# Optimization experiments

Measured on AMD Instinct MI355X. Metric: run time of the kernel, lower is better.

## Reference

```python
import jax, jax.numpy as jnp
import numpy as np

B, S, D, H = 2, 2048, 1024, 16
DK = D // H
MAX_REL = 2047          # clip range for relative distances
REL_DIM = 64            # rel_embedding dim, summed over


def setup_inputs() -> dict:
    key = jax.random.key(0)
    ks = jax.random.split(key, 12)
    sc = 1.0 / np.sqrt(D)
    inp = {
        "q": jax.random.normal(ks[0], (B, S, D), jnp.float32),
        "k": jax.random.normal(ks[1], (B, S, D), jnp.float32),
        "v": jax.random.normal(ks[2], (B, S, D), jnp.float32),
        "Wq": jax.random.normal(ks[3], (D, D), jnp.float32) * sc,
        "bq": jnp.zeros((D,), jnp.float32),
        "Wk": jax.random.normal(ks[4], (D, D), jnp.float32) * sc,
        "bk": jnp.zeros((D,), jnp.float32),
        "Wv": jax.random.normal(ks[5], (D, D), jnp.float32) * sc,
        "bv": jnp.zeros((D,), jnp.float32),
        "Wo": jax.random.normal(ks[6], (D, D), jnp.float32) * sc,
        "bo": jnp.zeros((D,), jnp.float32),
        "rel_table": jax.random.normal(ks[7], (2 * MAX_REL + 1, REL_DIM), jnp.float32) * 0.02,
        "mask": jnp.tril(jnp.ones((1, 1, S, S), jnp.bool_)),  # causal
    }
    return inp


def reference(q, k, v, Wq, bq, Wk, bk, Wv, bv, Wo, bo, rel_table, mask):
    def split_heads(x):
        # [B,S,D] -> [B,H,S,DK]
        return x.reshape(B, -1, H, DK).transpose(0, 2, 1, 3)

    Q = split_heads(q @ Wq + bq)
    K = split_heads(k @ Wk + bk)
    V = split_heads(v @ Wv + bv)

    scores = jnp.einsum("bhqd,bhkd->bhqk", Q, K) / jnp.sqrt(jnp.float32(DK))

    # relative position bias: table[clip(j - i)] summed over rel dim -> [S,S]
    rel_idx = jnp.clip(jnp.arange(S)[None, :] - jnp.arange(S)[:, None],
                       -MAX_REL, MAX_REL) + MAX_REL
    rel_bias = rel_table[rel_idx].sum(-1)  # [S,S]
    scores = scores + rel_bias[None, None]

    scores = jnp.where(mask, scores, jnp.float32(-1e20))
    attn = jax.nn.softmax(scores, axis=-1)

    out = jnp.einsum("bhqk,bhkd->bhqd", attn, V)
    out = out.transpose(0, 2, 1, 3).reshape(B, -1, D)
    return out @ Wo + bo
```

## Files before the change

### kernel.cpp

```cpp
#include <hip/hip_runtime.h>

#define SEQ 2048
#define DIM 1024
#define NH 16
#define HD 64
#define NB 2

typedef __bf16 bf16x8 __attribute__((ext_vector_type(8)));
typedef float f32x4 __attribute__((ext_vector_type(4)));
typedef float f32x4v __attribute__((ext_vector_type(4)));
typedef float f32x4u __attribute__((ext_vector_type(4), aligned(4)));
typedef unsigned short us8 __attribute__((ext_vector_type(8)));
typedef unsigned short us4 __attribute__((ext_vector_type(4)));

#define LOG2E 1.44269504f

__device__ __forceinline__ unsigned short bfbits(float f) {
  __bf16 h = (__bf16)f;
  return __builtin_bit_cast(unsigned short, h);
}

__global__ void relsum_kernel(const float* __restrict__ rel_table,
                              float* __restrict__ relsum) {
  int i = blockIdx.x * blockDim.x + threadIdx.x;
  if (i < 4095) {
    const f32x4v* row = reinterpret_cast<const f32x4v*>(rel_table + (size_t)i * 64);
    float s = 0.f;
    for (int d = 0; d < 16; ++d) {
      f32x4v v = row[d];
      s += v[0] + v[1] + v[2] + v[3];
    }
    relsum[i] = s * LOG2E;
  }
}

__global__ __launch_bounds__(256) void wconv4_kernel(
    const float* __restrict__ W0, const float* __restrict__ W1,
    const float* __restrict__ W2, const float* __restrict__ W3,
    unsigned short* __restrict__ Wt) {
  __shared__ unsigned short T[64][68];
  int z = blockIdx.z;
  const float* W = (z == 0) ? W0 : (z == 1) ? W1 : (z == 2) ? W2 : W3;
  unsigned short* out = Wt + (size_t)z * 1024 * 1024;
  int r0 = blockIdx.y * 64;
  int c0 = blockIdx.x * 64;
  int tid = threadIdx.x;
  for (int it = 0; it < 4; ++it) {
    int s = tid + it * 256;
    int r = s >> 4;
    int c4 = (s & 15) * 4;
    f32x4v v = *reinterpret_cast<const f32x4v*>(W + (size_t)(r0 + r) * 1024 + c0 + c4);
    us4 o;
    o[0] = bfbits(v[0]); o[1] = bfbits(v[1]); o[2] = bfbits(v[2]); o[3] = bfbits(v[3]);
    *reinterpret_cast<us4*>(&T[r][c4]) = o;
  }
  __syncthreads();
  for (int it = 0; it < 2; ++it) {
    int s = tid + it * 256;
    int n = s >> 3;
    int k8 = (s & 7) * 8;
    us8 o;
    for (int e = 0; e < 8; ++e) o[e] = T[k8 + e][n];
    *reinterpret_cast<us8*>(out + (size_t)(c0 + n) * 1024 + r0 + k8) = o;
  }
}

template <int A_BF16, int OUT_BF16>
__global__ __launch_bounds__(256) void gemm_bias_kernel(
    const void* __restrict__ Ap, const unsigned short* __restrict__ WT,
    const float* __restrict__ bias, void* __restrict__ Cp, float oscale) {
  constexpr int N = 1024, K = 1024;
  int o = ((blockIdx.x & 7) << 6) | (blockIdx.x >> 3);
  int col0 = (o & 15) * 64;
  int row0 = (o >> 4) * 128;
  int tid = threadIdx.x;
  int w = tid >> 6;
  int lane = tid & 63;
  int lg = lane >> 4;
  int li = lane & 15;
  int wr = (w >> 1) * 64;
  int wc = (w & 1) * 32;

  __shared__ unsigned short As[128][72];
  __shared__ unsigned short Ws[64][72];

  f32x4 acc[4][2] = {};

  for (int k0 = 0; k0 < K; k0 += 64) {
    __syncthreads();
    if (A_BF16) {
      const unsigned short* A = (const unsigned short*)Ap;
      for (int it = 0; it < 4; ++it) {
        int s = tid + it * 256;
        int r = s >> 3;
        int cg = (s & 7) * 8;
        us8 vv = *reinterpret_cast<const us8*>(A + (size_t)(row0 + r) * K + k0 + cg);
        *reinterpret_cast<us8*>(&As[r][cg]) = vv;
      }
    } else {
      const float* A = (const float*)Ap;
      for (int it = 0; it < 8; ++it) {
        int s = tid + it * 256;
        int r = s >> 4;
        int cg = (s & 15) * 4;
        f32x4v vv = *reinterpret_cast<const f32x4v*>(A + (size_t)(row0 + r) * K + k0 + cg);
        us4 o2;
        o2[0] = bfbits(vv[0]); o2[1] = bfbits(vv[1]); o2[2] = bfbits(vv[2]); o2[3] = bfbits(vv[3]);
        *reinterpret_cast<us4*>(&As[r][cg]) = o2;
      }
    }
    for (int it = 0; it < 2; ++it) {
      int s = tid + it * 256;
      int c = s >> 3;
      int kg = (s & 7) * 8;
      us8 vv = *reinterpret_cast<const us8*>(WT + (size_t)(col0 + c) * K + k0 + kg);
      *reinterpret_cast<us8*>(&Ws[c][kg]) = vv;
    }
    __syncthreads();
    for (int kk = 0; kk < 2; ++kk) {
      bf16x8 af[4], bfr[2];
      for (int m = 0; m < 4; ++m)
        af[m] = *reinterpret_cast<const bf16x8*>(&As[wr + m * 16 + li][kk * 32 + lg * 8]);
      for (int n = 0; n < 2; ++n)
        bfr[n] = *reinterpret_cast<const bf16x8*>(&Ws[wc + n * 16 + li][kk * 32 + lg * 8]);
      for (int m = 0; m < 4; ++m)
        for (int n = 0; n < 2; ++n)
          acc[m][n] = __builtin_amdgcn_mfma_f32_16x16x32_bf16(af[m], bfr[n], acc[m][n], 0, 0, 0);
    }
  }

  for (int m = 0; m < 4; ++m)
    for (int n = 0; n < 2; ++n)
      for (int r = 0; r < 4; ++r) {
        int row = row0 + wr + m * 16 + lg * 4 + r;
        int col = col0 + wc + n * 16 + li;
        float val = (acc[m][n][r] + bias[col]) * oscale;
        if (OUT_BF16)
          ((unsigned short*)Cp)[(size_t)row * N + col] = bfbits(val);
        else
          ((float*)Cp)[(size_t)row * N + col] = val;
      }
}

__global__ __launch_bounds__(256) void attn_kernel(
    const unsigned short* __restrict__ Qb, const unsigned short* __restrict__ Kb,
    const unsigned short* __restrict__ Vb, const float* __restrict__ relsum,
    unsigned short* __restrict__ Ob) {
  int o = ((blockIdx.x & 7) << 6) | (blockIdx.x >> 3);
  int p = o & 15;
  int h = (o >> 4) & 15;
  int b = o >> 8;

  int tid = threadIdx.x;
  int w = tid >> 6;
  int lane = tid & 63;
  int lg = lane >> 4;
  int li = lane & 15;

  __shared__ unsigned short Ks[64][72];
  __shared__ unsigned short VtF[64 * 72];
  __shared__ __bf16 Ps[4][16][72];

  int key0 = tid >> 3;
  int cg0 = (tid & 7) * 8;
  int j0 = tid & 7;
  const unsigned short* kptr = Kb + ((size_t)(b * SEQ + key0)) * DIM + h * HD + cg0;
  const unsigned short* vptr = Vb + ((size_t)(b * SEQ + key0)) * DIM + h * HD + cg0;

  us8 krg0, krg1, vrg0, vrg1;

#define LOAD_REGS(TT)                                                     \
  {                                                                       \
    size_t off = (size_t)(TT) * 64 * DIM;                                 \
    krg0 = *reinterpret_cast<const us8*>(kptr + off);                     \
    vrg0 = *reinterpret_cast<const us8*>(vptr + off);                     \
    krg1 = *reinterpret_cast<const us8*>(kptr + off + 32 * DIM);          \
    vrg1 = *reinterpret_cast<const us8*>(vptr + off + 32 * DIM);          \
  }

#define WRITE_TILE()                                                      \
  {                                                                       \
    *reinterpret_cast<us8*>(&Ks[key0][cg0]) = krg0;                       \
    *reinterpret_cast<us8*>(&Ks[key0 + 32][cg0]) = krg1;                  \
    for (int e = 0; e < 8; ++e) {                                         \
      VtF[((unsigned)((cg0 + e) * 72 + key0)) ^ ((unsigned)j0 << 3)] = vrg0[e]; \
      VtF[((unsigned)((cg0 + e) * 72 + key0 + 32)) ^ ((unsigned)j0 << 3)] = vrg1[e]; \
    }                                                                     \
  }

  LOAD_REGS(0);

  for (int ph = 0; ph < 2; ++ph) {
    int qt = ph ? p : (31 - p);

    int qrow = qt * 64 + w * 16 + li;
    const unsigned short* qb = Qb + ((size_t)(b * SEQ + qrow)) * DIM + h * HD;
    bf16x8 qa0 = *reinterpret_cast<const bf16x8*>(qb + lg * 8);
    bf16x8 qa1 = *reinterpret_cast<const bf16x8*>(qb + 32 + lg * 8);

    f32x4 o_acc[4] = {};
    float m_row[4], l_row[4];
    for (int r = 0; r < 4; ++r) { m_row[r] = -3e38f; l_row[r] = 0.f; }
    int i0 = qt * 64 + w * 16 + lg * 4;

    for (int t = 0; t <= qt; ++t) {
      __syncthreads();
      WRITE_TILE();
      __syncthreads();

      if (!(ph == 1 && t == qt)) {
        int nextT = (t < qt) ? (t + 1) : 0;
        LOAD_REGS(nextT);
      }

      f32x4 s_acc[4] = {};
      __builtin_amdgcn_s_setprio(1);
      for (int kk = 0; kk < 2; ++kk) {
        bf16x8 qa = kk ? qa1 : qa0;
        for (int n = 0; n < 4; ++n) {
          bf16x8 kb = *reinterpret_cast<const bf16x8*>(&Ks[n * 16 + li][kk * 32 + lg * 8]);
          s_acc[n] = __builtin_amdgcn_mfma_f32_16x16x32_bf16(qa, kb, s_acc[n], 0, 0, 0);
        }
      }
      __builtin_amdgcn_s_setprio(0);

      float tmax[4] = {-3e38f, -3e38f, -3e38f, -3e38f};
      int Cbase = (t - qt) * 64 - (w * 16 + lg * 4) + li + 2047;
      if (t == qt) {
        for (int n = 0; n < 4; ++n) {
          int Cn = Cbase + n * 16;
          f32x4u rel4 = *reinterpret_cast<const f32x4u*>(&relsum[Cn - 3]);
          for (int r = 0; r < 4; ++r) {
            float sv = s_acc[n][r] + rel4[3 - r];
            sv = (Cn - r > 2047) ? -1e30f : sv;
            s_acc[n][r] = sv;
            tmax[r] = fmaxf(tmax[r], sv);
          }
        }
      } else {
        for (int n = 0; n < 4; ++n) {
          int Cn = Cbase + n * 16;
          f32x4u rel4 = *reinterpret_cast<const f32x4u*>(&relsum[Cn - 3]);
          for (int r = 0; r < 4; ++r) {
            float sv = s_acc[n][r] + rel4[3 - r];
            s_acc[n][r] = sv;
            tmax[r] = fmaxf(tmax[r], sv);
          }
        }
      }

      bool okl = true;
      for (int r = 0; r < 4; ++r) okl &= (tmax[r] <= m_row[r] + 8.f);
      if (!__all(okl)) {
        for (int msk = 1; msk < 16; msk <<= 1)
          for (int r = 0; r < 4; ++r)
            tmax[r] = fmaxf(tmax[r], __shfl_xor(tmax[r], msk));
        for (int r = 0; r < 4; ++r) {
          float mn = fmaxf(m_row[r], tmax[r]);
          float al = exp2f(m_row[r] - mn);
          m_row[r] = mn;
          l_row[r] *= al;
          o_acc[0][r] *= al; o_acc[1][r] *= al;
          o_acc[2][r] *= al; o_acc[3][r] *= al;
        }
      }

      for (int n = 0; n < 4; ++n)
        for (int r = 0; r < 4; ++r) {
          float e = exp2f(s_acc[n][r] - m_row[r]);
          s_acc[n][r] = e;
          l_row[r] += e;
        }

      for (int n = 0; n < 4; ++n)
        for (int r = 0; r < 4; ++r)
          Ps[w][lg * 4 + r][n * 16 + li] = (__bf16)s_acc[n][r];
      asm volatile("s_waitcnt lgkmcnt(0)" ::: "memory");
      __builtin_amdgcn_sched_barrier(0);

      __builtin_amdgcn_s_setprio(1);
      for (int kk = 0; kk < 2; ++kk) {
        bf16x8 pa = *reinterpret_cast<const bf16x8*>(&Ps[w][li][kk * 32 + lg * 8]);
        for (int n = 0; n < 4; ++n) {
          int dk = n * 16 + li;
          unsigned idx = ((unsigned)(dk * 72 + kk * 32 + lg * 8)) ^
                         ((((unsigned)dk >> 3) & 7u) << 3);
          bf16x8 vb = *reinterpret_cast<const bf16x8*>(&VtF[idx]);
          o_acc[n] = __builtin_amdgcn_mfma_f32_16x16x32_bf16(pa, vb, o_acc[n], 0, 0, 0);
        }
      }
      __builtin_amdgcn_s_setprio(0);
    }

    for (int msk = 1; msk < 16; msk <<= 1)
      for (int r = 0; r < 4; ++r) l_row[r] += __shfl_xor(l_row[r], msk);
    float inv_l[4];
    for (int r = 0; r < 4; ++r) inv_l[r] = 1.f / l_row[r];
    for (int n = 0; n < 4; ++n)
      for (int r = 0; r < 4; ++r) {
        int row = i0 + r;
        int dk = n * 16 + li;
        Ob[((size_t)(b * SEQ + row)) * DIM + h * HD + dk] =
            bfbits(o_acc[n][r] * inv_l[r]);
      }
  }
#undef LOAD_REGS
#undef WRITE_TILE
}

extern "C" void kernel_launch(void* const* d_in, const int* in_sizes, int n_in,
                              void* d_out, int out_size, void* d_ws, size_t ws_size,
                              hipStream_t stream) {
  const float* q = (const float*)d_in[0];
  const float* k = (const float*)d_in[1];
  const float* v = (const float*)d_in[2];
  const float* Wq = (const float*)d_in[3];
  const float* bq = (const float*)d_in[4];
  const float* Wk = (const float*)d_in[5];
  const float* bk = (const float*)d_in[6];
  const float* Wv = (const float*)d_in[7];
  const float* bv = (const float*)d_in[8];
  const float* Wo = (const float*)d_in[9];
  const float* bo = (const float*)d_in[10];
  const float* rel = (const float*)d_in[11];

  char* ws = (char*)d_ws;
  const size_t MATB = (size_t)NB * SEQ * DIM * sizeof(unsigned short);
  const size_t WTE = (size_t)DIM * DIM;
  unsigned short* Qb = (unsigned short*)(ws);
  unsigned short* Kb = (unsigned short*)(ws + MATB);
  unsigned short* Vb = (unsigned short*)(ws + 2 * MATB);
  unsigned short* Ob = (unsigned short*)(ws + 3 * MATB);
  float* relsum = (float*)(ws + 4 * MATB);
  unsigned short* WT = (unsigned short*)(ws + 4 * MATB + 65536);

  relsum_kernel<<<16, 256, 0, stream>>>(rel, relsum);
  wconv4_kernel<<<dim3(16, 16, 4), 256, 0, stream>>>(Wq, Wk, Wv, Wo, WT);

  const float qscale = 0.125f * LOG2E;
  gemm_bias_kernel<0, 1><<<dim3(512), 256, 0, stream>>>((const void*)q, WT + 0 * WTE, bq, (void*)Qb, qscale);
  gemm_bias_kernel<0, 1><<<dim3(512), 256, 0, stream>>>((const void*)k, WT + 1 * WTE, bk, (void*)Kb, 1.0f);
  gemm_bias_kernel<0, 1><<<dim3(512), 256, 0, stream>>>((const void*)v, WT + 2 * WTE, bv, (void*)Vb, 1.0f);

  attn_kernel<<<dim3(512), 256, 0, stream>>>(Qb, Kb, Vb, relsum, Ob);

  gemm_bias_kernel<1, 0><<<dim3(512), 256, 0, stream>>>((const void*)Ob, WT + 3 * WTE, bo, d_out, 1.0f);
}
```

Before: 149.7 us.

## Double-buffer LDS in GEMM and attention, flatten attention phases, cache rel bias in LDS

The GEMM kernel now double-buffers its A and W tiles in shared memory and prefetches two k-steps ahead, so it needs one barrier per step instead of two. The attention kernel double-buffers its K/V tiles and merges the two causal-balanced query phases into one 33-step loop, which keeps the prefetch pipeline running across the phase switch. It also copies the relative-bias vector into LDS once per block instead of reading it from global memory every tile. The cost is extra shared memory per block, which may lower occupancy, plus more complex index logic at the phase transition.

New measurement: 154.8 us. +3.4%, slower.

```diff
diff --git a/kernel.cpp b/kernel.cpp
--- a/kernel.cpp
+++ b/kernel.cpp
@@ -81,52 +81,99 @@
   int wr = (w >> 1) * 64;
   int wc = (w & 1) * 32;
 
-  __shared__ unsigned short As[128][72];
-  __shared__ unsigned short Ws[64][72];
+  __shared__ unsigned short As[2][128][72];
+  __shared__ unsigned short Ws[2][64][72];
+
+  f32x4v af32[8];
+  us8 ab16[4];
+  us8 wreg[2];
+
+#define GLOADA(KS)                                                        \
+  {                                                                       \
+    int k0 = (KS) * 64;                                                   \
+    if (A_BF16) {                                                         \
+      const unsigned short* A = (const unsigned short*)Ap;                \
+      for (int it = 0; it < 4; ++it) {                                    \
+        int s = tid + it * 256;                                           \
+        int r = s >> 3;                                                   \
+        int cg = (s & 7) * 8;                                             \
+        ab16[it] = *reinterpret_cast<const us8*>(                         \
+            A + (size_t)(row0 + r) * K + k0 + cg);                        \
+      }                                                                   \
+    } else {                                                              \
+      const float* A = (const float*)Ap;                                  \
+      for (int it = 0; it < 8; ++it) {                                    \
+        int s = tid + it * 256;                                           \
+        int r = s >> 4;                                                   \
+        int cg = (s & 15) * 4;                                            \
+        af32[it] = *reinterpret_cast<const f32x4v*>(                      \
+            A + (size_t)(row0 + r) * K + k0 + cg);                        \
+      }                                                                   \
+    }                                                                     \
+  }
+
+#define GLOADW(KS)                                                        \
+  {                                                                       \
+    int k0 = (KS) * 64;                                                   \
+    for (int it = 0; it < 2; ++it) {                                      \
+      int s = tid + it * 256;                                             \
+      int c = s >> 3;                                                     \
+      int kg = (s & 7) * 8;                                               \
+      wreg[it] = *reinterpret_cast<const us8*>(                           \
+          WT + (size_t)(col0 + c) * K + k0 + kg);                         \
+    }                                                                     \
+  }
+
+#define SWRITE(B)                                                         \
+  {                                                                       \
+    if (A_BF16) {                                                         \
+      for (int it = 0; it < 4; ++it) {                                    \
+        int s = tid + it * 256;                                           \
+        int r = s >> 3;                                                   \
+        int cg = (s & 7) * 8;                                             \
+        *reinterpret_cast<us8*>(&As[B][r][cg]) = ab16[it];                \
+      }                                                                   \
+    } else {                                                              \
+      for (int it = 0; it < 8; ++it) {                                    \
+        int s = tid + it * 256;                                           \
+        int r = s >> 4;                                                   \
+        int cg = (s & 15) * 4;                                            \
+        us4 o2;                                                           \
+        o2[0] = bfbits(af32[it][0]); o2[1] = bfbits(af32[it][1]);         \
+        o2[2] = bfbits(af32[it][2]); o2[3] = bfbits(af32[it][3]);         \
+        *reinterpret_cast<us4*>(&As[B][r][cg]) = o2;                      \
+      }                                                                   \
+    }                                                                     \
+    for (int it = 0; it < 2; ++it) {                                      \
+      int s = tid + it * 256;                                             \
+      int c = s >> 3;                                                     \
+      int kg = (s & 7) * 8;                                               \
+      *reinterpret_cast<us8*>(&Ws[B][c][kg]) = wreg[it];                  \
+    }                                                                     \
+  }
 
   f32x4 acc[4][2] = {};
 
-  for (int k0 = 0; k0 < K; k0 += 64) {
-    __syncthreads();
-    if (A_BF16) {
-      const unsigned short* A = (const unsigned short*)Ap;
-      for (int it = 0; it < 4; ++it) {
-        int s = tid + it * 256;
-        int r = s >> 3;
-        int cg = (s & 7) * 8;
-        us8 vv = *reinterpret_cast<const us8*>(A + (size_t)(row0 + r) * K + k0 + cg);
-        *reinterpret_cast<us8*>(&As[r][cg]) = vv;
-      }
-    } else {
-      const float* A = (const float*)Ap;
-      for (int it = 0; it < 8; ++it) {
-        int s = tid + it * 256;
-        int r = s >> 4;
-        int cg = (s & 15) * 4;
-        f32x4v vv = *reinterpret_cast<const f32x4v*>(A + (size_t)(row0 + r) * K + k0 + cg);
-        us4 o2;
-        o2[0] = bfbits(vv[0]); o2[1] = bfbits(vv[1]); o2[2] = bfbits(vv[2]); o2[3] = bfbits(vv[3]);
-        *reinterpret_cast<us4*>(&As[r][cg]) = o2;
-      }
-    }
-    for (int it = 0; it < 2; ++it) {
-      int s = tid + it * 256;
-      int c = s >> 3;
-      int kg = (s & 7) * 8;
-      us8 vv = *reinterpret_cast<const us8*>(WT + (size_t)(col0 + c) * K + k0 + kg);
-      *reinterpret_cast<us8*>(&Ws[c][kg]) = vv;
-    }
-    __syncthreads();
+  GLOADA(0); GLOADW(0);
+  SWRITE(0);
+  GLOADA(1); GLOADW(1);
+  __syncthreads();
+
+  for (int ks = 0; ks < 16; ++ks) {
+    if (ks < 15) SWRITE((ks + 1) & 1);
+    if (ks < 14) { GLOADA(ks + 2); GLOADW(ks + 2); }
+    int B = ks & 1;
     for (int kk = 0; kk < 2; ++kk) {
       bf16x8 af[4], bfr[2];
       for (int m = 0; m < 4; ++m)
-        af[m] = *reinterpret_cast<const bf16x8*>(&As[wr + m * 16 + li][kk * 32 + lg * 8]);
+        af[m] = *reinterpret_cast<const bf16x8*>(&As[B][wr + m * 16 + li][kk * 32 + lg * 8]);
       for (int n = 0; n < 2; ++n)
-        bfr[n] = *reinterpret_cast<const bf16x8*>(&Ws[wc + n * 16 + li][kk * 32 + lg * 8]);
+        bfr[n] = *reinterpret_cast<const bf16x8*>(&Ws[B][wc + n * 16 + li][kk * 32 + lg * 8]);
       for (int m = 0; m < 4; ++m)
         for (int n = 0; n < 2; ++n)
           acc[m][n] = __builtin_amdgcn_mfma_f32_16x16x32_bf16(af[m], bfr[n], acc[m][n], 0, 0, 0);
     }
+    __syncthreads();
   }
 
   for (int m = 0; m < 4; ++m)
@@ -140,6 +187,9 @@
         else
           ((float*)Cp)[(size_t)row * N + col] = val;
       }
+#undef GLOADA
+#undef GLOADW
+#undef SWRITE
 }
 
 __global__ __launch_bounds__(256) void attn_kernel(
@@ -157,9 +207,17 @@
   int lg = lane >> 4;
   int li = lane & 15;
 
-  __shared__ unsigned short Ks[64][72];
-  __shared__ unsigned short VtF[64 * 72];
+  __shared__ unsigned short Ks[2][64][72];
+  __shared__ unsigned short VtF[2][64 * 72];
   __shared__ __bf16 Ps[4][16][72];
+  __shared__ float rel_lds[2112];
+
+  for (int it = 0; it < 3; ++it) {
+    int slot = tid + it * 256;
+    if (slot < 528)
+      *reinterpret_cast<f32x4v*>(&rel_lds[slot * 4]) =
+          *reinterpret_cast<const f32x4v*>(&relsum[slot * 4]);
+  }
 
   int key0 = tid >> 3;
   int cg0 = (tid & 7) * 8;
@@ -178,131 +236,150 @@
     vrg1 = *reinterpret_cast<const us8*>(vptr + off + 32 * DIM);          \
   }
 
-#define WRITE_TILE()                                                      \
+#define WRITE_TILE(B)                                                     \
   {                                                                       \
-    *reinterpret_cast<us8*>(&Ks[key0][cg0]) = krg0;                       \
-    *reinterpret_cast<us8*>(&Ks[key0 + 32][cg0]) = krg1;                  \
+    *reinterpret_cast<us8*>(&Ks[B][key0][cg0]) = krg0;                    \
+    *reinterpret_cast<us8*>(&Ks[B][key0 + 32][cg0]) = krg1;               \
     for (int e = 0; e < 8; ++e) {                                         \
-      VtF[((unsigned)((cg0 + e) * 72 + key0)) ^ ((unsigned)j0 << 3)] = vrg0[e]; \
-      VtF[((unsigned)((cg0 + e) * 72 + key0 + 32)) ^ ((unsigned)j0 << 3)] = vrg1[e]; \
+      VtF[B][((unsigned)((cg0 + e) * 72 + key0)) ^ ((unsigned)j0 << 3)] = vrg0[e]; \
+      VtF[B][((unsigned)((cg0 + e) * 72 + key0 + 32)) ^ ((unsigned)j0 << 3)] = vrg1[e]; \
     }                                                                     \
   }
 
+  int qt0 = 31 - p;
+
   LOAD_REGS(0);
-
-  for (int ph = 0; ph < 2; ++ph) {
-    int qt = ph ? p : (31 - p);
-
-    int qrow = qt * 64 + w * 16 + li;
-    const unsigned short* qb = Qb + ((size_t)(b * SEQ + qrow)) * DIM + h * HD;
-    bf16x8 qa0 = *reinterpret_cast<const bf16x8*>(qb + lg * 8);
-    bf16x8 qa1 = *reinterpret_cast<const bf16x8*>(qb + 32 + lg * 8);
-
-    f32x4 o_acc[4] = {};
-    float m_row[4], l_row[4];
-    for (int r = 0; r < 4; ++r) { m_row[r] = -3e38f; l_row[r] = 0.f; }
-    int i0 = qt * 64 + w * 16 + lg * 4;
-
-    for (int t = 0; t <= qt; ++t) {
-      __syncthreads();
-      WRITE_TILE();
-      __syncthreads();
-
-      if (!(ph == 1 && t == qt)) {
-        int nextT = (t < qt) ? (t + 1) : 0;
-        LOAD_REGS(nextT);
-      }
-
-      f32x4 s_acc[4] = {};
-      __builtin_amdgcn_s_setprio(1);
-      for (int kk = 0; kk < 2; ++kk) {
-        bf16x8 qa = kk ? qa1 : qa0;
-        for (int n = 0; n < 4; ++n) {
-          bf16x8 kb = *reinterpret_cast<const bf16x8*>(&Ks[n * 16 + li][kk * 32 + lg * 8]);
-          s_acc[n] = __builtin_amdgcn_mfma_f32_16x16x32_bf16(qa, kb, s_acc[n], 0, 0, 0);
+  WRITE_TILE(0);
+  LOAD_REGS(1);
+
+  int qrow = qt0 * 64 + w * 16 + li;
+  const unsigned short* qb = Qb + ((size_t)(b * SEQ + qrow)) * DIM + h * HD;
+  bf16x8 qa0 = *reinterpret_cast<const bf16x8*>(qb + lg * 8);
+  bf16x8 qa1 = *reinterpret_cast<const bf16x8*>(qb + 32 + lg * 8);
+
+  f32x4 o_acc[4] = {};
+  float m_row[4], l_row[4];
+  for (int r = 0; r < 4; ++r) { m_row[r] = -3e38f; l_row[r] = 0.f; }
+  int qt = qt0;
+  int tshift = 0;
+  int i0 = qt0 * 64 + w * 16 + lg * 4;
+
+  __syncthreads();
+
+  for (int s = 0; s <= 32; ++s) {
+    if (s < 32) WRITE_TILE((s + 1) & 1);
+    if (s < 31) {
+      int t2 = (s + 2 <= qt0) ? (s + 2) : (s + 1 - qt0);
+      LOAD_REGS(t2);
+    }
+    int t = s - tshift;
+    int B = s & 1;
+
+    f32x4 s_acc[4] = {};
+    __builtin_amdgcn_s_setprio(1);
+    for (int kk = 0; kk < 2; ++kk) {
+      bf16x8 qa = kk ? qa1 : qa0;
+      for (int n = 0; n < 4; ++n) {
+        bf16x8 kb = *reinterpret_cast<const bf16x8*>(&Ks[B][n * 16 + li][kk * 32 + lg * 8]);
+        s_acc[n] = __builtin_amdgcn_mfma_f32_16x16x32_bf16(qa, kb, s_acc[n], 0, 0, 0);
+      }
+    }
+    __builtin_amdgcn_s_setprio(0);
+
+    float tmax[4] = {-3e38f, -3e38f, -3e38f, -3e38f};
+    int Cbase = (t - qt) * 64 - (w * 16 + lg * 4) + li + 2047;
+    bool diag = (t == qt);
+    if (diag) {
+      for (int n = 0; n < 4; ++n) {
+        int Cn = Cbase + n * 16;
+        f32x4u rel4 = *reinterpret_cast<const f32x4u*>(&rel_lds[Cn - 3]);
+        for (int r = 0; r < 4; ++r) {
+          float sv = s_acc[n][r] + rel4[3 - r];
+          sv = (Cn - r > 2047) ? -1e30f : sv;
+          s_acc[n][r] = sv;
+          tmax[r] = fmaxf(tmax[r], sv);
         }
       }
-      __builtin_amdgcn_s_setprio(0);
-
-      float tmax[4] = {-3e38f, -3e38f, -3e38f, -3e38f};
-      int Cbase = (t - qt) * 64 - (w * 16 + lg * 4) + li + 2047;
-      if (t == qt) {
-        for (int n = 0; n < 4; ++n) {
-          int Cn = Cbase + n * 16;
-          f32x4u rel4 = *reinterpret_cast<const f32x4u*>(&relsum[Cn - 3]);
-          for (int r = 0; r < 4; ++r) {
-            float sv = s_acc[n][r] + rel4[3 - r];
-            sv = (Cn - r > 2047) ? -1e30f : sv;
-            s_acc[n][r] = sv;
-            tmax[r] = fmaxf(tmax[r], sv);
-          }
+    } else {
+      for (int n = 0; n < 4; ++n) {
+        int Cn = Cbase + n * 16;
+        f32x4u rel4 = *reinterpret_cast<const f32x4u*>(&rel_lds[Cn - 3]);
+        for (int r = 0; r < 4; ++r) {
+          float sv = s_acc[n][r] + rel4[3 - r];
+          s_acc[n][r] = sv;
+          tmax[r] = fmaxf(tmax[r], sv);
         }
-      } else {
-        for (int n = 0; n < 4; ++n) {
-          int Cn = Cbase + n * 16;
-          f32x4u rel4 = *reinterpret_cast<const f32x4u*>(&relsum[Cn - 3]);
-          for (int r = 0; r < 4; ++r) {
-            float sv = s_acc[n][r] + rel4[3 - r];
-            s_acc[n][r] = sv;
-            tmax[r] = fmaxf(tmax[r], sv);
-          }
-        }
-      }
-
-      bool okl = true;
-      for (int r = 0; r < 4; ++r) okl &= (tmax[r] <= m_row[r] + 8.f);
-      if (!__all(okl)) {
-        for (int msk = 1; msk < 16; msk <<= 1)
-          for (int r = 0; r < 4; ++r)
-            tmax[r] = fmaxf(tmax[r], __shfl_xor(tmax[r], msk));
-        for (int r = 0; r < 4; ++r) {
-          float mn = fmaxf(m_row[r], tmax[r]);
-          float al = exp2f(m_row[r] - mn);
-          m_row[r] = mn;
-          l_row[r] *= al;
-          o_acc[0][r] *= al; o_acc[1][r] *= al;
-          o_acc[2][r] *= al; o_acc[3][r] *= al;
-        }
-      }
-
+      }
+    }
+
+    bool okl = true;
+    for (int r = 0; r < 4; ++r) okl &= (tmax[r] <= m_row[r] + 8.f);
+    if (!__all(okl)) {
+      for (int msk = 1; msk < 16; msk <<= 1)
+        for (int r = 0; r < 4; ++r)
+          tmax[r] = fmaxf(tmax[r], __shfl_xor(tmax[r], msk));
+      for (int r = 0; r < 4; ++r) {
+        float mn = fmaxf(m_row[r], tmax[r]);
+        float al = exp2f(m_row[r] - mn);
+        m_row[r] = mn;
+        l_row[r] *= al;
+        o_acc[0][r] *= al; o_acc[1][r] *= al;
+        o_acc[2][r] *= al; o_acc[3][r] *= al;
+      }
+    }
+
+    for (int n = 0; n < 4; ++n)
+      for (int r = 0; r < 4; ++r) {
+        float e = exp2f(s_acc[n][r] - m_row[r]);
+        s_acc[n][r] = e;
+        l_row[r] += e;
+      }
+
+    for (int n = 0; n < 4; ++n)
+      for (int r = 0; r < 4; ++r)
+        Ps[w][lg * 4 + r][n * 16 + li] = (__bf16)s_acc[n][r];
+    asm volatile("s_waitcnt lgkmcnt(0)" ::: "memory");
+    __builtin_amdgcn_sched_barrier(0);
+
+    __builtin_amdgcn_s_setprio(1);
+    for (int kk = 0; kk < 2; ++kk) {
+      bf16x8 pa = *reinterpret_cast<const bf16x8*>(&Ps[w][li][kk * 32 + lg * 8]);
+      for (int n = 0; n < 4; ++n) {
+        int dk = n * 16 + li;
+        unsigned idx = ((unsigned)(dk * 72 + kk * 32 + lg * 8)) ^
+                       ((((unsigned)dk >> 3) & 7u) << 3);
+        bf16x8 vb = *reinterpret_cast<const bf16x8*>(&VtF[B][idx]);
+        o_acc[n] = __builtin_amdgcn_mfma_f32_16x16x32_bf16(pa, vb, o_acc[n], 0, 0, 0);
+      }
+    }
+    __builtin_amdgcn_s_setprio(0);
+
+    if (t == qt) {
+      for (int msk = 1; msk < 16; msk <<= 1)
+        for (int r = 0; r < 4; ++r) l_row[r] += __shfl_xor(l_row[r], msk);
+      float inv_l[4];
+      for (int r = 0; r < 4; ++r) inv_l[r] = 1.f / l_row[r];
       for (int n = 0; n < 4; ++n)
         for (int r = 0; r < 4; ++r) {
-          float e = exp2f(s_acc[n][r] - m_row[r]);
-          s_acc[n][r] = e;
-          l_row[r] += e;
+          int row = i0 + r;
+          int dk = n * 16 + li;
+          Ob[((size_t)(b * SEQ + row)) * DIM + h * HD + dk] =
+              bfbits(o_acc[n][r] * inv_l[r]);
         }
-
-      for (int n = 0; n < 4; ++n)
-        for (int r = 0; r < 4; ++r)
-          Ps[w][lg * 4 + r][n * 16 + li] = (__bf16)s_acc[n][r];
-      asm volatile("s_waitcnt lgkmcnt(0)" ::: "memory");
-      __builtin_amdgcn_sched_barrier(0);
-
-      __builtin_amdgcn_s_setprio(1);
-      for (int kk = 0; kk < 2; ++kk) {
-        bf16x8 pa = *reinterpret_cast<const bf16x8*>(&Ps[w][li][kk * 32 + lg * 8]);
-        for (int n = 0; n < 4; ++n) {
-          int dk = n * 16 + li;
-          unsigned idx = ((unsigned)(dk * 72 + kk * 32 + lg * 8)) ^
-                         ((((unsigned)dk >> 3) & 7u) << 3);
-          bf16x8 vb = *reinterpret_cast<const bf16x8*>(&VtF[idx]);
-          o_acc[n] = __builtin_amdgcn_mfma_f32_16x16x32_bf16(pa, vb, o_acc[n], 0, 0, 0);
-        }
-      }
-      __builtin_amdgcn_s_setprio(0);
-    }
-
-    for (int msk = 1; msk < 16; msk <<= 1)
-      for (int r = 0; r < 4; ++r) l_row[r] += __shfl_xor(l_row[r], msk);
-    float inv_l[4];
-    for (int r = 0; r < 4; ++r) inv_l[r] = 1.f / l_row[r];
-    for (int n = 0; n < 4; ++n)
-      for (int r = 0; r < 4; ++r) {
-        int row = i0 + r;
-        int dk = n * 16 + li;
-        Ob[((size_t)(b * SEQ + row)) * DIM + h * HD + dk] =
-            bfbits(o_acc[n][r] * inv_l[r]);
-      }
+      if (s < 32) {
+        qt = p;
+        tshift = qt0 + 1;
+        qrow = p * 64 + w * 16 + li;
+        qb = Qb + ((size_t)(b * SEQ + qrow)) * DIM + h * HD;
+        qa0 = *reinterpret_cast<const bf16x8*>(qb + lg * 8);
+        qa1 = *reinterpret_cast<const bf16x8*>(qb + 32 + lg * 8);
+        for (int r = 0; r < 4; ++r) { m_row[r] = -3e38f; l_row[r] = 0.f; }
+        for (int n = 0; n < 4; ++n)
+          for (int r = 0; r < 4; ++r) o_acc[n][r] = 0.f;
+        i0 = p * 64 + w * 16 + lg * 4;
+      }
+    }
+    __syncthreads();
   }
 #undef LOAD_REGS
 #undef WRITE_TILE
```
